# Optimization experiments

Hardware: AMD Instinct MI355X
Metric: run time of the kernel (lower is better)

## Reference

```python
import jax, jax.numpy as jnp
import numpy as np

N = 40          # grid side
DT = 1.0        # time step
LEAKY = 0.03    # leaky rate


def setup_inputs() -> dict:
    key = jax.random.key(0)
    k1, = jax.random.split(key, 1)
    n = N
    c0, dc, crr, CN = 300.0, -250.0 / n, 0.8, 0.1
    # replicate the torch init: column-dependent wave speed with random relative perturbation
    c = c0 * jnp.ones((n, n), jnp.float32) + dc * (jnp.arange(n, dtype=jnp.float32) - 1.0)[None, :]
    c = c - crr * jax.random.uniform(k1, (n, n), jnp.float32) * c
    dx = (DT / CN) * jnp.max(c) * np.float32(np.sqrt(2.0)) * jnp.ones((n, n), jnp.float32)
    return {
        "c": c,
        "k": jnp.zeros((n, n), jnp.float32),
        "kp": 1e-4 * jnp.ones((n, n), jnp.float32),
        "dx": dx,
        "dy": dx,
    }


def reference(c, k, kp, dx, dy):
    n = N
    g = n * n                      # grid_size
    s = 3 * g                      # state_size
    sp = jax.nn.softplus
    c_pos = sp(c).reshape(-1)      # [g]
    k_x = sp(k).reshape(-1)        # [g] (k_y identical in original)
    kp_p = sp(kp).reshape(-1)      # [g]
    # dx, dy are passed but unused by the eigendecomposition (faithful to source)

    xi = jnp.float32(np.pi / 2.0)  # xi_magnitude = pi / (2*1.0)
    lam1 = 1.0 / (1.0 + DT * k_x)                                   # [g] real
    real_part = 0.5 * (1.0 / (1.0 + DT * kp_p) + lam1)
    imag_part = c_pos * DT * xi / jnp.sqrt((1.0 + DT * kp_p) * (1.0 + DT * k_x))
    lam2 = (real_part + 1j * imag_part).astype(jnp.complex64)
    lam3 = jnp.conj(lam2)
    Lambda = jnp.concatenate([lam1.astype(jnp.complex64), lam2, lam3])  # [3g]

    beta = DT / (1.0 + DT * k_x)
    alpha = lam2 - lam1.astype(jnp.complex64) + 1e-6
    v2 = (beta.astype(jnp.complex64) * 1j * xi) / alpha   # v2_2 == v2_3
    v3 = -jnp.conj(v2)                                    # v3_2 == v3_3

    ones_c = jnp.ones(g, jnp.complex64)
    Z = jnp.zeros((g, g), jnp.complex64)
    D = jnp.diag
    # block-diagonal-structured eigenvector matrix, [3g, 3g]
    P = jnp.block([
        [D(ones_c), D(ones_c), D(ones_c)],
        [Z,         D(v2),     D(v3)],
        [Z,         D(v2),     D(v3)],
    ])
    # A = Re(P @ diag(Lambda) @ P^H); P @ diag(L) is column scaling
    A = ((P * Lambda[None, :]) @ jnp.conj(P).T).real
    W = (A - (1.0 - LEAKY) * jnp.eye(s, dtype=A.dtype)) / LEAKY
    return (A, W, c_pos.reshape(n, n), k)
```

## Files before the change

kernel.cpp:

```cpp
#include <hip/hip_runtime.h>
#include <math.h>


constexpr int   GN  = 40;
constexpr int   G   = GN * GN;
constexpr long long S  = 3LL * G;
constexpr long long SS = S * S;

__global__ void zero_fill_kernel(float4* __restrict__ out, long long n4) {
    long long i      = (long long)blockIdx.x * blockDim.x + threadIdx.x;
    long long stride = (long long)gridDim.x * blockDim.x;
    const float4 z = make_float4(0.f, 0.f, 0.f, 0.f);
    for (; i < n4; i += stride) out[i] = z;
}

__device__ __forceinline__ float softplus_f(float x) {
    return fmaxf(x, 0.0f) + log1pf(expf(-fabsf(x)));
}

__global__ void eigen_scatter_kernel(const float* __restrict__ c,
                                     const float* __restrict__ k,
                                     const float* __restrict__ kp,
                                     float* __restrict__ out) {
    int i = blockIdx.x * blockDim.x + threadIdx.x;
    if (i >= G) return;

    float cv  = c[i];
    float kv  = k[i];
    float kpv = kp[i];

    float c_pos = softplus_f(cv);
    float k_x   = softplus_f(kv);
    float kp_p  = softplus_f(kpv);

    const float xi = 1.57079632679489662f;

    float okx  = 1.0f + k_x;
    float okp  = 1.0f + kp_p;
    float lam1 = 1.0f / okx;
    float rp   = 0.5f * (1.0f / okp + lam1);
    float im   = c_pos * xi / sqrtf(okp * okx);

    float ar   = rp - lam1 + 1e-6f;
    float bx   = lam1 * xi;
    float den  = ar * ar + im * im;
    float v2sq = bx * bx / den;

    float d1 = lam1 + 2.0f * rp;
    float d2 = 2.0f * v2sq * rp;

    float* __restrict__ A = out;
    float* __restrict__ W = out + SS;

    long long di0 = (long long)i            * (S + 1);
    long long di1 = (long long)(G + i)      * (S + 1);
    long long di2 = (long long)(2 * G + i)  * (S + 1);

    A[di0]     = d1;
    A[di1]     = d2;
    A[di1 + G] = d2;
    A[di2 - G] = d2;
    A[di2]     = d2;

    const float LEAKY = 0.03f;
    const float OML   = 0.97f;
    W[di0]     = (d1 - OML) / LEAKY;
    W[di1]     = (d2 - OML) / LEAKY;
    W[di1 + G] = d2 / LEAKY;
    W[di2 - G] = d2 / LEAKY;
    W[di2]     = (d2 - OML) / LEAKY;

    out[2 * SS + i]     = c_pos;
    out[2 * SS + G + i] = kv;
}

extern "C" void kernel_launch(void* const* d_in, const int* in_sizes, int n_in,
                              void* d_out, int out_size, void* d_ws, size_t ws_size,
                              hipStream_t stream) {
    const float* c  = (const float*)d_in[0];
    const float* k  = (const float*)d_in[1];
    const float* kp = (const float*)d_in[2];
    float* out = (float*)d_out;

    long long n4 = (2LL * SS) / 4;
    zero_fill_kernel<<<2048, 256, 0, stream>>>((float4*)out, n4);

    eigen_scatter_kernel<<<(G + 255) / 256, 256, 0, stream>>>(c, k, kp, out);
}
```

Measured before the change: 39.14 us.

## Fuse zero-fill and diagonal scatter into one row-wise write kernel

New measurement: 32.73 us (median of 2 runs). 16.4% less time.

```diff
diff --git a/kernel.cpp b/kernel.cpp
--- a/kernel.cpp
+++ b/kernel.cpp
@@ -2,76 +2,79 @@
 #include <math.h>
 
 
-constexpr int   GN  = 40;
-constexpr int   G   = GN * GN;
-constexpr long long S  = 3LL * G;
-constexpr long long SS = S * S;
-
-__global__ void zero_fill_kernel(float4* __restrict__ out, long long n4) {
-    long long i      = (long long)blockIdx.x * blockDim.x + threadIdx.x;
-    long long stride = (long long)gridDim.x * blockDim.x;
-    const float4 z = make_float4(0.f, 0.f, 0.f, 0.f);
-    for (; i < n4; i += stride) out[i] = z;
-}
+constexpr int       GN = 40;
+constexpr int       G  = GN * GN;
+constexpr int       S  = 3 * G;
+constexpr long long SS = (long long)S * S;
+constexpr int       ROW4 = S / 4;
 
 __device__ __forceinline__ float softplus_f(float x) {
     return fmaxf(x, 0.0f) + log1pf(expf(-fabsf(x)));
 }
 
-__global__ void eigen_scatter_kernel(const float* __restrict__ c,
-                                     const float* __restrict__ k,
-                                     const float* __restrict__ kp,
-                                     float* __restrict__ out) {
-    int i = blockIdx.x * blockDim.x + threadIdx.x;
-    if (i >= G) return;
+__global__ __launch_bounds__(256) void eigen_rows_kernel(
+        const float* __restrict__ c,
+        const float* __restrict__ k,
+        const float* __restrict__ kp,
+        float* __restrict__ out) {
+    int r = blockIdx.x;
 
-    float cv  = c[i];
-    float kv  = k[i];
-    float kpv = kp[i];
+    if (r >= 2 * S) {
+        for (int i = threadIdx.x; i < G; i += 256) {
+            out[2 * SS + i]     = softplus_f(c[i]);
+            out[2 * SS + G + i] = k[i];
+        }
+        return;
+    }
 
-    float c_pos = softplus_f(cv);
-    float k_x   = softplus_f(kv);
-    float kp_p  = softplus_f(kpv);
+    bool isW = r >= S;
+    int  rr  = isW ? r - S : r;
+    int  b   = rr / G;
+    int  g   = rr % G;
+
+    float c_pos = softplus_f(c[g]);
+    float k_x   = softplus_f(k[g]);
+    float kp_p  = softplus_f(kp[g]);
 
     const float xi = 1.57079632679489662f;
-
     float okx  = 1.0f + k_x;
     float okp  = 1.0f + kp_p;
     float lam1 = 1.0f / okx;
     float rp   = 0.5f * (1.0f / okp + lam1);
     float im   = c_pos * xi / sqrtf(okp * okx);
-
     float ar   = rp - lam1 + 1e-6f;
     float bx   = lam1 * xi;
-    float den  = ar * ar + im * im;
-    float v2sq = bx * bx / den;
+    float v2sq = bx * bx / (ar * ar + im * im);
 
     float d1 = lam1 + 2.0f * rp;
     float d2 = 2.0f * v2sq * rp;
 
-    float* __restrict__ A = out;
-    float* __restrict__ W = out + SS;
+    const float INV_L = 1.0f / 0.03f;
+    const float OML   = 0.97f;
 
-    long long di0 = (long long)i            * (S + 1);
-    long long di1 = (long long)(G + i)      * (S + 1);
-    long long di2 = (long long)(2 * G + i)  * (S + 1);
+    int   c1, c2;
+    float v1, v2v;
+    if (b == 0) {
+        c1 = g;      v1 = isW ? (d1 - OML) * INV_L : d1;
+        c2 = -1;     v2v = 0.0f;
+    } else if (b == 1) {
+        c1 = G + g;      v1  = isW ? (d2 - OML) * INV_L : d2;
+        c2 = 2 * G + g;  v2v = isW ? d2 * INV_L : d2;
+    } else {
+        c1 = G + g;      v1  = isW ? d2 * INV_L : d2;
+        c2 = 2 * G + g;  v2v = isW ? (d2 - OML) * INV_L : d2;
+    }
 
-    A[di0]     = d1;
-    A[di1]     = d2;
-    A[di1 + G] = d2;
-    A[di2 - G] = d2;
-    A[di2]     = d2;
-
-    const float LEAKY = 0.03f;
-    const float OML   = 0.97f;
-    W[di0]     = (d1 - OML) / LEAKY;
-    W[di1]     = (d2 - OML) / LEAKY;
-    W[di1 + G] = d2 / LEAKY;
-    W[di2 - G] = d2 / LEAKY;
-    W[di2]     = (d2 - OML) / LEAKY;
-
-    out[2 * SS + i]     = c_pos;
-    out[2 * SS + G + i] = kv;
+    float4* __restrict__ row4 = (float4*)out + (long long)r * ROW4;
+    for (int i4 = threadIdx.x; i4 < ROW4; i4 += 256) {
+        int c0 = i4 * 4;
+        float4 v;
+        v.x = (c0     == c1) ? v1 : ((c0     == c2) ? v2v : 0.0f);
+        v.y = (c0 + 1 == c1) ? v1 : ((c0 + 1 == c2) ? v2v : 0.0f);
+        v.z = (c0 + 2 == c1) ? v1 : ((c0 + 2 == c2) ? v2v : 0.0f);
+        v.w = (c0 + 3 == c1) ? v1 : ((c0 + 3 == c2) ? v2v : 0.0f);
+        row4[i4] = v;
+    }
 }
 
 extern "C" void kernel_launch(void* const* d_in, const int* in_sizes, int n_in,
@@ -82,8 +85,5 @@
     const float* kp = (const float*)d_in[2];
     float* out = (float*)d_out;
 
-    long long n4 = (2LL * SS) / 4;
-    zero_fill_kernel<<<2048, 256, 0, stream>>>((float4*)out, n4);
-
-    eigen_scatter_kernel<<<(G + 255) / 256, 256, 0, stream>>>(c, k, kp, out);
+    eigen_rows_kernel<<<2 * S + 1, 256, 0, stream>>>(c, k, kp, out);
 }
```
